# Performance work log

Hardware: AMD Instinct MI355X
Metric: run time of the kernel (lower is better)

The kernel has to match this reference:

```python
import jax, jax.numpy as jnp
import numpy as np

N_TH1 = 33
N_TH2 = 2 * (N_TH1 - 1) + 1
LB, UB = 1e-20, 1e20
LB_EXP, UB_EXP = -20.0, 20.0


def _make_directions():
    # Spherical direction grid, matching the TF constructor loop order.
    th1 = np.linspace(-np.pi / 2, np.pi / 2, N_TH1)
    th2 = np.linspace(-np.pi, np.pi, N_TH2)
    c1, s1 = np.cos(th1), np.sin(th1)
    c2, s2 = np.cos(th2), np.sin(th2)
    i = np.arange(1, N_TH1 - 1)
    j = np.arange(N_TH2 - 1)
    dx = np.outer(c1[i], c2[j]).ravel()
    dy = np.outer(c1[i], s2[j]).ravel()
    dz = np.repeat(s1[i], len(j))
    d = np.stack([dx, dy, dz], axis=-1)
    poles = np.array([[c1[0] * c2[0], c1[0] * s2[0], s1[0]],
                      [c1[-1] * c2[0], c1[-1] * s2[0], s1[-1]]])
    return jnp.asarray(np.concatenate([d, poles], 0), jnp.float32)  # [D,3]


def _spt(dirs, local_v, smoothness, trans):
    # dirs [D,3], local_v [B,P,V,3], smoothness [B,P], trans [B,P,1,3]
    z = jnp.einsum('bpvc,dc->bpvd', local_v, dirs)            # [B,P,V,D]
    zm = jnp.where(z > 0, z, 0.0)
    p = smoothness[:, :, None, None]                          # [B,P,1,1]
    # Overflow-safe exponent scaling: pick k=10^ceil(lk) so max(zm*k)^p >= 1e-20.
    zm_log = jnp.log10(jnp.max(zm, axis=2, keepdims=True))    # [B,P,1,D]
    exponent = zm_log * p
    lk = jnp.where(exponent < LB_EXP, (LB_EXP - exponent) / p, 0.0)
    k = jnp.power(10.0, jnp.clip(jnp.ceil(lk), 0.0, UB_EXP))  # [B,P,1,D]
    k = jax.lax.stop_gradient(k)  # ceil has zero grad in the original too
    zms = zm * k
    pos = zms > 0
    # clip(zm^p, LB, UB) - (zm==0)*LB  ==  where(zm>0, clip(zm^p,LB,UB), 0)
    zm_p = jnp.where(pos, jnp.clip(jnp.where(pos, zms, 1.0) ** p, LB, UB), 0.0)
    sum_zm_p = jnp.sum(zm_p, axis=2, keepdims=True)           # [B,P,1,D]
    h = jnp.clip(sum_zm_p ** (1.0 / p), LB, UB)               # [B,P,1,D]
    ratio = jnp.where(pos, zms, 1.0) / h
    dhdz = jnp.where(pos, jnp.clip(ratio ** (p - 1.0), LB, UB), LB)  # [B,P,V,D]
    surf = jnp.einsum('bpvd,bpvc->bpdc', dhdz, local_v) + trans      # [B,P,D,3]
    h_out = jnp.transpose(jnp.clip(h / k, -UB, UB), (0, 1, 3, 2))    # [B,P,D,1]
    return h_out, surf


def setup_inputs() -> dict:
    key = jax.random.key(0)
    k1, k2 = jax.random.split(key)
    vertices = jax.random.normal(k1, (8, 16, 64, 3), dtype=jnp.float32)
    # smoothness p in [2, 20] (positive power-norm exponent)
    smoothness = 2.0 + 18.0 * jax.random.uniform(k2, (8, 16), dtype=jnp.float32)
    return {'vertices': vertices, 'smoothness': smoothness}


def reference(vertices, smoothness):
    dirs = _make_directions()                                 # [D,3]
    mean_v = jnp.mean(vertices, axis=2, keepdims=True)        # [B,P,1,3]
    local_v = vertices - mean_v
    h, surf = _spt(dirs, local_v, smoothness, mean_v)
    B, P = vertices.shape[0], vertices.shape[1]
    D = dirs.shape[0]
    local_dirs = jnp.broadcast_to(dirs, (B, P, D, 3))
    direction_h = jnp.concatenate([local_dirs, h], axis=-1)   # [B,P,D,4]
    points = surf.reshape(B, P * D, 3)                        # [B, P*D, 3]
    overlap = jnp.zeros((B, P, 1), jnp.float32)               # overlap routine truncated in source
    mean_out = mean_v.reshape(B, P, 3)
    return (points, direction_h, overlap, mean_out, dirs, local_v)
```

## Files before the change

### kernel.cpp

```cpp
#include <hip/hip_runtime.h>

#define NB 8
#define NP 16
#define NV 64
#define ND 1986

#define OFF_POINTS 0
#define OFF_DH     762624
#define OFF_OVER   1779456
#define OFF_MEAN   1779584
#define OFF_DIRS   1779968
#define OFF_LOCALV 1785926

__global__ __launch_bounds__(256, 4) void mcx_kernel(
    const float* __restrict__ verts,
    const float* __restrict__ smooth,
    float* __restrict__ out)
{
    const int t     = threadIdx.x;
    const int bp    = blockIdx.x >> 3;
    const int chunk = blockIdx.x & 7;
    const int d     = chunk * 256 + t;

    __shared__ float lv[NV][4];
    __shared__ float mean_sh[3];

    const int v3 = t / 3;
    const int c3 = t - v3 * 3;
    if (t < 192) lv[v3][c3] = verts[bp * 192 + t];
    else         lv[t - 192][3] = 0.f;
    __syncthreads();
    if (t < 3) {
        float s = 0.f;
        for (int v = 0; v < NV; ++v) s += lv[v][t];
        mean_sh[t] = s * (1.f / 64.f);
    }
    __syncthreads();
    const float m0 = mean_sh[0], m1 = mean_sh[1], m2 = mean_sh[2];
    if (t < 192) lv[v3][c3] -= mean_sh[c3];
    __syncthreads();

    if (chunk == 0) {
        if (t < 192) out[OFF_LOCALV + bp * 192 + t] = lv[v3][c3];
        if (t < 3)   out[OFF_MEAN + bp * 3 + t] = mean_sh[t];
        if (t == 3)  out[OFF_OVER + bp] = 0.f;
    }

    if (d >= ND) return;

    int i, j;
    if (d < 1984) { i = 1 + (d >> 6); j = d & 63; }
    else          { i = (d == 1984) ? 0 : 32; j = 0; }
    const double STEP = 3.141592653589793 / 32.0;
    const float th1 = (float)(-1.5707963267948966 + (double)i * STEP);
    const float th2 = (float)(-3.141592653589793  + (double)j * STEP);
    const float c1 = cosf(th1), s1 = sinf(th1);
    const float c2 = cosf(th2), s2 = sinf(th2);
    const float dx = c1 * c2, dy = c1 * s2, dz = s1;
    if (bp == 0) {
        out[OFF_DIRS + d * 3 + 0] = dx;
        out[OFF_DIRS + d * 3 + 1] = dy;
        out[OFF_DIRS + d * 3 + 2] = dz;
    }

    const float sm  = smooth[bp];
    const float ip  = 1.0f / sm;
    const float pm1 = sm - 1.0f;

    float zv[NV];
    float zmax = 0.f;
    #pragma unroll
    for (int v = 0; v < NV; ++v) {
        float z = fmaf(lv[v][0], dx, fmaf(lv[v][1], dy, lv[v][2] * dz));
        zv[v] = z;
        zmax = fmaxf(zmax, z);
    }

    const float zlog = log10f(zmax);
    const float expo = zlog * sm;
    const float lk   = (expo < -20.f) ? ((-20.f - expo) / sm) : 0.f;
    const float kc   = fminf(fmaxf(ceilf(lk), 0.f), 20.f);
    const float k    = exp2f(kc * 3.3219280948873623f);

    float sum = 0.f;
    #pragma unroll
    for (int v = 0; v < NV; ++v) {
        float zms = fmaxf(zv[v], 0.f) * k;
        float lz  = log2f(zms);
        zv[v] = lz;
        float t2 = exp2f(sm * lz);
        t2 = fminf(fmaxf(t2, 1e-20f), 1e20f);
        sum += (zms > 0.f) ? t2 : 0.f;
    }

    const float h  = fminf(fmaxf(exp2f(ip * log2f(sum)), 1e-20f), 1e20f);
    const float lh = log2f(h);

    float sx = 0.f, sy = 0.f, sz = 0.f;
    #pragma unroll
    for (int v = 0; v < NV; ++v) {
        float e  = pm1 * (zv[v] - lh);
        float dh = fminf(fmaxf(exp2f(e), 1e-20f), 1e20f);
        sx = fmaf(dh, lv[v][0], sx);
        sy = fmaf(dh, lv[v][1], sy);
        sz = fmaf(dh, lv[v][2], sz);
    }

    const int idx = bp * ND + d;
    out[OFF_POINTS + idx * 3 + 0] = sx + m0;
    out[OFF_POINTS + idx * 3 + 1] = sy + m1;
    out[OFF_POINTS + idx * 3 + 2] = sz + m2;

    const float hout = fminf(h / k, 1e20f);
    out[OFF_DH + idx * 4 + 0] = dx;
    out[OFF_DH + idx * 4 + 1] = dy;
    out[OFF_DH + idx * 4 + 2] = dz;
    out[OFF_DH + idx * 4 + 3] = hout;
}

extern "C" void kernel_launch(void* const* d_in, const int* in_sizes, int n_in,
                              void* d_out, int out_size, void* d_ws, size_t ws_size,
                              hipStream_t stream) {
    const float* verts  = (const float*)d_in[0];
    const float* smooth = (const float*)d_in[1];
    float* out = (float*)d_out;
    (void)d_ws; (void)ws_size; (void)in_sizes; (void)n_in; (void)out_size;
    mcx_kernel<<<dim3(NB * NP * 8), dim3(256), 0, stream>>>(verts, smooth, out);
}
```

Measured before the change: 76.43 us.

## Split vertices across thread pairs and normalize by max instead of power-of-ten scaling

Each direction is now handled by two threads, each covering 32 vertices, with max, sum and the xyz accumulators combined through xor shuffles. The 10^k overflow-safe scaling is replaced by dividing by the max projection in log space, and the clamps and zero checks are dropped in favour of fast __log2f. This doubles the grid and halves per-thread register arrays to raise parallelism and cut transcendental work. The output stores are split between the two threads. The risk is numerical divergence from the reference's clamping semantics, for example in the LB/UB clamps and in how zero projections are handled.

```diff
diff --git a/kernel.cpp b/kernel.cpp
--- a/kernel.cpp
+++ b/kernel.cpp
@@ -18,9 +18,11 @@
     float* __restrict__ out)
 {
     const int t     = threadIdx.x;
-    const int bp    = blockIdx.x >> 3;
-    const int chunk = blockIdx.x & 7;
-    const int d     = chunk * 256 + t;
+    const int bp    = blockIdx.x >> 4;
+    const int chunk = blockIdx.x & 15;
+    const int dl    = t >> 1;
+    const int half  = t & 1;
+    const int d     = chunk * 128 + dl;
 
     __shared__ float lv[NV][4];
     __shared__ float mean_sh[3];
@@ -57,7 +59,7 @@
     const float c1 = cosf(th1), s1 = sinf(th1);
     const float c2 = cosf(th2), s2 = sinf(th2);
     const float dx = c1 * c2, dy = c1 * s2, dz = s1;
-    if (bp == 0) {
+    if (bp == 0 && half == 0) {
         out[OFF_DIRS + d * 3 + 0] = dx;
         out[OFF_DIRS + d * 3 + 1] = dy;
         out[OFF_DIRS + d * 3 + 2] = dz;
@@ -66,56 +68,58 @@
     const float sm  = smooth[bp];
     const float ip  = 1.0f / sm;
     const float pm1 = sm - 1.0f;
+    const int voff  = half * 32;
 
-    float zv[NV];
-    float zmax = 0.f;
+    float zv[32];
+    float m = 0.f;
     #pragma unroll
-    for (int v = 0; v < NV; ++v) {
-        float z = fmaf(lv[v][0], dx, fmaf(lv[v][1], dy, lv[v][2] * dz));
+    for (int v = 0; v < 32; ++v) {
+        const float* q = lv[voff + v];
+        float z = fmaf(q[0], dx, fmaf(q[1], dy, q[2] * dz));
+        z = fmaxf(z, 0.f);
         zv[v] = z;
-        zmax = fmaxf(zmax, z);
+        m = fmaxf(m, z);
     }
-
-    const float zlog = log10f(zmax);
-    const float expo = zlog * sm;
-    const float lk   = (expo < -20.f) ? ((-20.f - expo) / sm) : 0.f;
-    const float kc   = fminf(fmaxf(ceilf(lk), 0.f), 20.f);
-    const float k    = exp2f(kc * 3.3219280948873623f);
+    m = fmaxf(m, __shfl_xor(m, 1, 64));
+    m = fmaxf(m, 1e-37f);
+    const float lm = __log2f(m);
 
     float sum = 0.f;
     #pragma unroll
-    for (int v = 0; v < NV; ++v) {
-        float zms = fmaxf(zv[v], 0.f) * k;
-        float lz  = log2f(zms);
+    for (int v = 0; v < 32; ++v) {
+        float lz = __log2f(zv[v]) - lm;
         zv[v] = lz;
-        float t2 = exp2f(sm * lz);
-        t2 = fminf(fmaxf(t2, 1e-20f), 1e20f);
-        sum += (zms > 0.f) ? t2 : 0.f;
+        sum += exp2f(sm * lz);
     }
-
-    const float h  = fminf(fmaxf(exp2f(ip * log2f(sum)), 1e-20f), 1e20f);
-    const float lh = log2f(h);
+    sum += __shfl_xor(sum, 1, 64);
+    const float lh = ip * __log2f(fmaxf(sum, 1e-30f));
 
     float sx = 0.f, sy = 0.f, sz = 0.f;
     #pragma unroll
-    for (int v = 0; v < NV; ++v) {
-        float e  = pm1 * (zv[v] - lh);
-        float dh = fminf(fmaxf(exp2f(e), 1e-20f), 1e20f);
-        sx = fmaf(dh, lv[v][0], sx);
-        sy = fmaf(dh, lv[v][1], sy);
-        sz = fmaf(dh, lv[v][2], sz);
+    for (int v = 0; v < 32; ++v) {
+        float dh = exp2f(pm1 * (zv[v] - lh));
+        const float* q = lv[voff + v];
+        sx = fmaf(dh, q[0], sx);
+        sy = fmaf(dh, q[1], sy);
+        sz = fmaf(dh, q[2], sz);
     }
+    sx += __shfl_xor(sx, 1, 64);
+    sy += __shfl_xor(sy, 1, 64);
+    sz += __shfl_xor(sz, 1, 64);
+
+    const float hout = m * exp2f(lh);
 
     const int idx = bp * ND + d;
-    out[OFF_POINTS + idx * 3 + 0] = sx + m0;
-    out[OFF_POINTS + idx * 3 + 1] = sy + m1;
-    out[OFF_POINTS + idx * 3 + 2] = sz + m2;
-
-    const float hout = fminf(h / k, 1e20f);
-    out[OFF_DH + idx * 4 + 0] = dx;
-    out[OFF_DH + idx * 4 + 1] = dy;
-    out[OFF_DH + idx * 4 + 2] = dz;
-    out[OFF_DH + idx * 4 + 3] = hout;
+    if (half == 0) {
+        out[OFF_POINTS + idx * 3 + 0] = sx + m0;
+        out[OFF_POINTS + idx * 3 + 1] = sy + m1;
+        out[OFF_POINTS + idx * 3 + 2] = sz + m2;
+    } else {
+        out[OFF_DH + idx * 4 + 0] = dx;
+        out[OFF_DH + idx * 4 + 1] = dy;
+        out[OFF_DH + idx * 4 + 2] = dz;
+        out[OFF_DH + idx * 4 + 3] = hout;
+    }
 }
 
 extern "C" void kernel_launch(void* const* d_in, const int* in_sizes, int n_in,
@@ -125,5 +129,5 @@
     const float* smooth = (const float*)d_in[1];
     float* out = (float*)d_out;
     (void)d_ws; (void)ws_size; (void)in_sizes; (void)n_in; (void)out_size;
-    mcx_kernel<<<dim3(NB * NP * 8), dim3(256), 0, stream>>>(verts, smooth, out);
+    mcx_kernel<<<dim3(NB * NP * 16), dim3(256), 0, stream>>>(verts, smooth, out);
 }
```

Measured after the change: 72.62 us. -5.0%, faster.
